# Kernel tuning notes

Hardware: AMD Instinct MI355X
Metric: run time of the kernel (lower is better)

Reference implementation:

```python
import jax, jax.numpy as jnp
import numpy as np

NUM_USERS = 100000
NUM_ITEMS = 200000
EMB_DIM = 64
N_LAYERS = 3
NNZ = 10000000
BATCH = 8192
N = NUM_USERS + NUM_ITEMS


def setup_inputs() -> dict:
    key = jax.random.key(0)
    k = jax.random.split(key, 7)
    return {
        "user_emb": jax.random.normal(k[0], (NUM_USERS, EMB_DIM), dtype=jnp.float32) * 0.05,
        "item_emb": jax.random.normal(k[1], (NUM_ITEMS, EMB_DIM), dtype=jnp.float32) * 0.05,
        "adj_vals": jax.random.uniform(k[2], (NNZ,), dtype=jnp.float32) * 0.01,
        "adj_rows": jax.random.randint(k[3], (NNZ,), 0, N, dtype=jnp.int32),
        "adj_cols": jax.random.randint(k[4], (NNZ,), 0, N, dtype=jnp.int32),
        "u_idx": jax.random.randint(k[5], (BATCH,), 0, NUM_USERS, dtype=jnp.int32),
        "i_idx": jax.random.randint(k[6], (BATCH,), 0, NUM_ITEMS, dtype=jnp.int32),
    }


def reference(user_emb, item_emb, adj_vals, adj_rows, adj_cols, u_idx, i_idx):
    # x0: [N, d] stacked user+item embeddings
    x0 = jnp.concatenate([user_emb, item_emb], axis=0)
    acc = x0
    x = x0
    for _ in range(N_LAYERS):
        # SpMM via gather + scaled scatter-add: y[r] += v * x[c]
        msg = adj_vals[:, None] * x[adj_cols]          # [nnz, d]
        x = jax.ops.segment_sum(msg, adj_rows, num_segments=N)
        acc = acc + x
    out = acc / jnp.float32(N_LAYERS + 1)              # mean over layer outputs
    u_all = out[:NUM_USERS]
    i_all = out[NUM_USERS:]
    # score(u_idx, i_idx): dot product of gathered final embeddings
    return jnp.sum(u_all[u_idx] * i_all[i_idx], axis=-1)  # [BATCH]
```

## Files before the change

kernel.cpp:

```cpp
#include <hip/hip_runtime.h>

#define NUM_USERS 100000
#define NUM_ITEMS 200000
#define EMB_DIM   64
#define NNODES    (NUM_USERS + NUM_ITEMS)
#define NNZ_C     10000000
#define BATCH_C   8192

typedef unsigned long long u64;

__device__ __forceinline__ u64 pack_edge(int c, float v) {
    return (u64)(unsigned int)c | ((u64)__float_as_uint(v) << 32);
}

__device__ __forceinline__ unsigned short f2bf(float f) {
    unsigned u = __float_as_uint(f);
    u += 0x7fffu + ((u >> 16) & 1u);
    return (unsigned short)(u >> 16);
}
__device__ __forceinline__ float bf2f(unsigned short h) {
    return __uint_as_float((unsigned)h << 16);
}

__global__ void zero_int_kernel(int* __restrict__ p, int n) {
    int i = blockIdx.x * blockDim.x + threadIdx.x;
    if (i < n) p[i] = 0;
}

__global__ void zero_f32_kernel(float* __restrict__ p, long long n) {
    long long i = (long long)blockIdx.x * blockDim.x + threadIdx.x;
    long long stride = (long long)gridDim.x * blockDim.x;
    for (; i < n; i += stride) p[i] = 0.f;
}

__global__ void convert_x0_kernel(const float* __restrict__ uemb,
                                  const float* __restrict__ iemb,
                                  ushort* __restrict__ x0) {
    const long long total4 = (long long)NNODES * EMB_DIM / 4;
    const long long usr4   = (long long)NUM_USERS * EMB_DIM / 4;
    long long g = (long long)blockIdx.x * blockDim.x + threadIdx.x;
    long long stride = (long long)gridDim.x * blockDim.x;
    for (; g < total4; g += stride) {
        long long base = g * 4;
        const float* src = (g < usr4) ? (uemb + base)
                                      : (iemb + (base - (long long)NUM_USERS * EMB_DIM));
        float4 v = *reinterpret_cast<const float4*>(src);
        ushort4 o = make_ushort4(f2bf(v.x), f2bf(v.y), f2bf(v.z), f2bf(v.w));
        *reinterpret_cast<ushort4*>(x0 + base) = o;
    }
}

__global__ void hist_kernel(const int* __restrict__ rows, int* __restrict__ cnt) {
    int i = blockIdx.x * blockDim.x + threadIdx.x;
    int stride = gridDim.x * blockDim.x;
    for (; i < NNZ_C; i += stride) {
        atomicAdd(&cnt[__builtin_nontemporal_load(rows + i)], 1);
    }
}

__global__ void scan_a(const int* __restrict__ cnt, int* __restrict__ rp,
                       int* __restrict__ bsum) {
    __shared__ int sm[256];
    int t = threadIdx.x;
    int base = blockIdx.x * 1024 + t * 4;
    int v0 = (base + 0 < NNODES) ? cnt[base + 0] : 0;
    int v1 = (base + 1 < NNODES) ? cnt[base + 1] : 0;
    int v2 = (base + 2 < NNODES) ? cnt[base + 2] : 0;
    int v3 = (base + 3 < NNODES) ? cnt[base + 3] : 0;
    int s = v0 + v1 + v2 + v3;
    sm[t] = s;
    __syncthreads();
    for (int off = 1; off < 256; off <<= 1) {
        int val = (t >= off) ? sm[t - off] : 0;
        __syncthreads();
        sm[t] += val;
        __syncthreads();
    }
    int incl = sm[t];
    int excl = incl - s;
    if (base + 0 < NNODES) rp[base + 0] = excl;
    if (base + 1 < NNODES) rp[base + 1] = excl + v0;
    if (base + 2 < NNODES) rp[base + 2] = excl + v0 + v1;
    if (base + 3 < NNODES) rp[base + 3] = excl + v0 + v1 + v2;
    if (t == 255) bsum[blockIdx.x] = incl;
}

__global__ void scan_b(int* __restrict__ bsum, int nblk) {
    __shared__ int sm[512];
    int t = threadIdx.x;
    int v = (t < nblk) ? bsum[t] : 0;
    sm[t] = v;
    __syncthreads();
    for (int off = 1; off < 512; off <<= 1) {
        int val = (t >= off) ? sm[t - off] : 0;
        __syncthreads();
        sm[t] += val;
        __syncthreads();
    }
    int excl = sm[t] - v;
    if (t < nblk) bsum[t] = excl;
}

__global__ void scan_c(int* __restrict__ rp, const int* __restrict__ bsum,
                       int* __restrict__ cursor) {
    int i = blockIdx.x * blockDim.x + threadIdx.x;
    if (i < NNODES) {
        int v = rp[i] + bsum[i >> 10];
        rp[i] = v;
        cursor[i] = v;
    }
    if (i == 0) rp[NNODES] = NNZ_C;
}

__global__ void scatter_kernel(const int* __restrict__ rows,
                               const int* __restrict__ cols,
                               const float* __restrict__ vals,
                               int* __restrict__ cursor,
                               u64* __restrict__ ccv) {
    int i = blockIdx.x * blockDim.x + threadIdx.x;
    int stride = gridDim.x * blockDim.x;
    for (; i < NNZ_C; i += stride) {
        int r = __builtin_nontemporal_load(rows + i);
        int c = __builtin_nontemporal_load(cols + i);
        float v = __builtin_nontemporal_load(vals + i);
        int pos = atomicAdd(&cursor[r], 1);
        ccv[pos] = pack_edge(c, v);
    }
}

template <bool ACCUM>
__global__ __launch_bounds__(256) void spmm_bf_kernel(
        const int* __restrict__ row_ptr, const u64* __restrict__ ccv,
        const ushort* __restrict__ xin, ushort* __restrict__ xout) {
    int row = blockIdx.x * 16 + (threadIdx.x >> 4);
    int lane = threadIdx.x & 63;
    int dl = lane & 15;
    int base = lane & 48;

    int start = row_ptr[row];
    int end   = row_ptr[row + 1];

    float ax = 0.f, ay = 0.f, az = 0.f, aw = 0.f;

    int cur = start;
    for (; cur + 16 <= end; cur += 16) {
        u64 e = __builtin_nontemporal_load(ccv + cur + dl);
        int   c = (int)(unsigned int)(e & 0xffffffffu);
        float v = __uint_as_float((unsigned int)(e >> 32));
#pragma unroll
        for (int j = 0; j < 16; ++j) {
            int   cj = __shfl(c, base + j);
            float vj = __shfl(v, base + j);
            ushort4 xb = *reinterpret_cast<const ushort4*>(
                xin + (size_t)cj * EMB_DIM + dl * 4);
            ax += vj * bf2f(xb.x);
            ay += vj * bf2f(xb.y);
            az += vj * bf2f(xb.z);
            aw += vj * bf2f(xb.w);
        }
    }
    int n = end - cur;
    if (n > 0) {
        int   c = 0;
        float v = 0.f;
        if (dl < n) {
            u64 e = ccv[cur + dl];
            c = (int)(unsigned int)(e & 0xffffffffu);
            v = __uint_as_float((unsigned int)(e >> 32));
        }
        for (int j = 0; j < n; ++j) {
            int   cj = __shfl(c, base + j);
            float vj = __shfl(v, base + j);
            ushort4 xb = *reinterpret_cast<const ushort4*>(
                xin + (size_t)cj * EMB_DIM + dl * 4);
            ax += vj * bf2f(xb.x);
            ay += vj * bf2f(xb.y);
            az += vj * bf2f(xb.z);
            aw += vj * bf2f(xb.w);
        }
    }

    ushort4* o = reinterpret_cast<ushort4*>(xout + (size_t)row * EMB_DIM) + dl;
    if (ACCUM) {
        ushort4 old = *o;
        ax += bf2f(old.x); ay += bf2f(old.y); az += bf2f(old.z); aw += bf2f(old.w);
    }
    *o = make_ushort4(f2bf(ax), f2bf(ay), f2bf(az), f2bf(aw));
}

template <bool FIRST>
__global__ __launch_bounds__(256) void coo_spmm_kernel(
        const int* __restrict__ rows, const int* __restrict__ cols,
        const float* __restrict__ vals, const float* __restrict__ xin,
        const float* __restrict__ uemb, const float* __restrict__ iemb,
        float* __restrict__ xout) {
    long long e = (long long)blockIdx.x * 16 + (threadIdx.x >> 4);
    int dl = threadIdx.x & 15;
    if (e >= NNZ_C) return;
    int r = rows[e];
    int c = cols[e];
    float v = vals[e];
    const float* src;
    if (FIRST) {
        src = (c < NUM_USERS) ? (uemb + (size_t)c * EMB_DIM)
                              : (iemb + (size_t)(c - NUM_USERS) * EMB_DIM);
    } else {
        src = xin + (size_t)c * EMB_DIM;
    }
    float4 xv = *reinterpret_cast<const float4*>(src + dl * 4);
    float* dst = xout + (size_t)r * EMB_DIM + dl * 4;
    atomicAdd(dst + 0, v * xv.x);
    atomicAdd(dst + 1, v * xv.y);
    atomicAdd(dst + 2, v * xv.z);
    atomicAdd(dst + 3, v * xv.w);
}

__global__ __launch_bounds__(256) void dot_bf_kernel(
        const float* __restrict__ uemb, const float* __restrict__ iemb,
        const ushort* __restrict__ A, const ushort* __restrict__ B,
        const int* __restrict__ u_idx, const int* __restrict__ i_idx,
        float* __restrict__ out) {
    int t = blockIdx.x * blockDim.x + threadIdx.x;
    int b = t >> 4;
    int dl = t & 15;
    if (b >= BATCH_C) return;

    int u = u_idx[b];
    int ii = i_idx[b];
    size_t uoff  = (size_t)u * EMB_DIM + dl * 4;
    size_t ioff  = (size_t)ii * EMB_DIM + dl * 4;
    size_t Aioff = (size_t)(NUM_USERS + ii) * EMB_DIM + dl * 4;

    float4 e_u = *reinterpret_cast<const float4*>(uemb + uoff);
    float4 e_i = *reinterpret_cast<const float4*>(iemb + ioff);
    ushort4 a_u = *reinterpret_cast<const ushort4*>(A + uoff);
    ushort4 b_u = *reinterpret_cast<const ushort4*>(B + uoff);
    ushort4 a_i = *reinterpret_cast<const ushort4*>(A + Aioff);
    ushort4 b_i = *reinterpret_cast<const ushort4*>(B + Aioff);

    float ux = e_u.x + bf2f(a_u.x) + bf2f(b_u.x);
    float uy = e_u.y + bf2f(a_u.y) + bf2f(b_u.y);
    float uz = e_u.z + bf2f(a_u.z) + bf2f(b_u.z);
    float uw = e_u.w + bf2f(a_u.w) + bf2f(b_u.w);
    float ix = e_i.x + bf2f(a_i.x) + bf2f(b_i.x);
    float iy = e_i.y + bf2f(a_i.y) + bf2f(b_i.y);
    float iz = e_i.z + bf2f(a_i.z) + bf2f(b_i.z);
    float iw = e_i.w + bf2f(a_i.w) + bf2f(b_i.w);

    float s = ux * ix + uy * iy + uz * iz + uw * iw;
    s += __shfl_xor(s, 1);
    s += __shfl_xor(s, 2);
    s += __shfl_xor(s, 4);
    s += __shfl_xor(s, 8);
    if (dl == 0) out[b] = s * 0.0625f;
}

__global__ __launch_bounds__(256) void dot_f32_kernel(
        const float* __restrict__ uemb, const float* __restrict__ iemb,
        const float* __restrict__ A, const float* __restrict__ B,
        const int* __restrict__ u_idx, const int* __restrict__ i_idx,
        float* __restrict__ out) {
    int t = blockIdx.x * blockDim.x + threadIdx.x;
    int b = t >> 4;
    int dl = t & 15;
    if (b >= BATCH_C) return;

    int u = u_idx[b];
    int ii = i_idx[b];
    size_t uoff  = (size_t)u * EMB_DIM + dl * 4;
    size_t ioff  = (size_t)ii * EMB_DIM + dl * 4;
    size_t Aioff = (size_t)(NUM_USERS + ii) * EMB_DIM + dl * 4;

    float4 e_u = *reinterpret_cast<const float4*>(uemb + uoff);
    float4 a_u = *reinterpret_cast<const float4*>(A + uoff);
    float4 b_u = *reinterpret_cast<const float4*>(B + uoff);
    float4 e_i = *reinterpret_cast<const float4*>(iemb + ioff);
    float4 a_i = *reinterpret_cast<const float4*>(A + Aioff);
    float4 b_i = *reinterpret_cast<const float4*>(B + Aioff);

    float ux = e_u.x + a_u.x + b_u.x, uy = e_u.y + a_u.y + b_u.y;
    float uz = e_u.z + a_u.z + b_u.z, uw = e_u.w + a_u.w + b_u.w;
    float ix = e_i.x + a_i.x + b_i.x, iy = e_i.y + a_i.y + b_i.y;
    float iz = e_i.z + a_i.z + b_i.z, iw = e_i.w + a_i.w + b_i.w;

    float s = ux * ix + uy * iy + uz * iz + uw * iw;
    s += __shfl_xor(s, 1);
    s += __shfl_xor(s, 2);
    s += __shfl_xor(s, 4);
    s += __shfl_xor(s, 8);
    if (dl == 0) out[b] = s * 0.0625f;
}

extern "C" void kernel_launch(void* const* d_in, const int* in_sizes, int n_in,
                              void* d_out, int out_size, void* d_ws, size_t ws_size,
                              hipStream_t stream) {
    const float* uemb     = (const float*)d_in[0];
    const float* iemb     = (const float*)d_in[1];
    const float* adj_vals = (const float*)d_in[2];
    const int*   adj_rows = (const int*)d_in[3];
    const int*   adj_cols = (const int*)d_in[4];
    const int*   u_idx    = (const int*)d_in[5];
    const int*   i_idx    = (const int*)d_in[6];
    float* out = (float*)d_out;
    (void)in_sizes; (void)n_in; (void)out_size;

    const size_t DENSE_BF = (size_t)NNODES * EMB_DIM * 2;
    const size_t DENSE_F32 = (size_t)NNODES * EMB_DIM * 4;
    const size_t ALIGN  = 256;
    auto rnd = [&](size_t b) { return (b + ALIGN - 1) & ~(ALIGN - 1); };

    const size_t need_full = rnd(DENSE_BF) * 3 + rnd((size_t)NNZ_C * 8) +
                             rnd((size_t)(NNODES + 1) * 4) + rnd((size_t)NNODES * 4) +
                             rnd(1024 * 4);
    const size_t need_min  = rnd(DENSE_F32) * 2;

    const long long dense_elems = (long long)NNODES * EMB_DIM;
    const int dot_grid = (BATCH_C * 16 + 255) / 256;

    if (ws_size >= need_full) {
        size_t off = 0;
        auto alloc = [&](size_t bytes) -> void* {
            void* p = (char*)d_ws + off;
            off += rnd(bytes);
            return p;
        };
        ushort* X0      = (ushort*)alloc(DENSE_BF);
        ushort* A       = (ushort*)alloc(DENSE_BF);
        ushort* B       = (ushort*)alloc(DENSE_BF);
        u64*    ccv     = (u64*)   alloc((size_t)NNZ_C * 8);
        int*    row_ptr = (int*)   alloc((size_t)(NNODES + 1) * 4);
        int*    cursor  = (int*)   alloc((size_t)NNODES * 4);
        int*    bsum    = (int*)   alloc(1024 * 4);

        const int nblk_scan = (NNODES + 1023) / 1024;

        zero_int_kernel<<<(NNODES + 255) / 256, 256, 0, stream>>>(cursor, NNODES);
        convert_x0_kernel<<<2048, 256, 0, stream>>>(uemb, iemb, X0);
        hist_kernel<<<2048, 256, 0, stream>>>(adj_rows, cursor);
        scan_a<<<nblk_scan, 256, 0, stream>>>(cursor, row_ptr, bsum);
        scan_b<<<1, 512, 0, stream>>>(bsum, nblk_scan);
        scan_c<<<(NNODES + 255) / 256, 256, 0, stream>>>(row_ptr, bsum, cursor);
        scatter_kernel<<<2048, 256, 0, stream>>>(adj_rows, adj_cols, adj_vals,
                                                 cursor, ccv);

        const int spmm_grid = NNODES / 16;
        spmm_bf_kernel<false><<<spmm_grid, 256, 0, stream>>>(row_ptr, ccv, X0, A);
        spmm_bf_kernel<false><<<spmm_grid, 256, 0, stream>>>(row_ptr, ccv, A, B);
        spmm_bf_kernel<true ><<<spmm_grid, 256, 0, stream>>>(row_ptr, ccv, B, A);

        dot_bf_kernel<<<dot_grid, 256, 0, stream>>>(uemb, iemb, A, B, u_idx, i_idx, out);
    } else if (ws_size >= need_min) {
        float* A = (float*)d_ws;
        float* B = (float*)((char*)d_ws + rnd(DENSE_F32));
        const int coo_grid = (NNZ_C + 15) / 16;

        zero_f32_kernel<<<2048, 256, 0, stream>>>(A, dense_elems);
        coo_spmm_kernel<true ><<<coo_grid, 256, 0, stream>>>(adj_rows, adj_cols, adj_vals,
                                                             nullptr, uemb, iemb, A);
        zero_f32_kernel<<<2048, 256, 0, stream>>>(B, dense_elems);
        coo_spmm_kernel<false><<<coo_grid, 256, 0, stream>>>(adj_rows, adj_cols, adj_vals,
                                                             A, nullptr, nullptr, B);
        coo_spmm_kernel<false><<<coo_grid, 256, 0, stream>>>(adj_rows, adj_cols, adj_vals,
                                                             B, nullptr, nullptr, A);

        dot_f32_kernel<<<dot_grid, 256, 0, stream>>>(uemb, iemb, A, B, u_idx, i_idx, out);
    }
}
```

Measured before the change: 1.650 ms.

## Build CSR via two-level bucketed counting sort with partitioned bucket counters

```diff
diff --git a/kernel.cpp b/kernel.cpp
--- a/kernel.cpp
+++ b/kernel.cpp
@@ -7,11 +7,13 @@
 #define NNZ_C     10000000
 #define BATCH_C   8192
 
+#define NBUCK     4688
+#define NPART     8
+#define NSEG      (NBUCK * NPART)
+#define SCAT_GRID 2048
+#define SCAN_ITEMS 37
+
 typedef unsigned long long u64;
-
-__device__ __forceinline__ u64 pack_edge(int c, float v) {
-    return (u64)(unsigned int)c | ((u64)__float_as_uint(v) << 32);
-}
 
 __device__ __forceinline__ unsigned short f2bf(float f) {
     unsigned u = __float_as_uint(f);
@@ -26,7 +28,6 @@
     int i = blockIdx.x * blockDim.x + threadIdx.x;
     if (i < n) p[i] = 0;
 }
-
 __global__ void zero_f32_kernel(float* __restrict__ p, long long n) {
     long long i = (long long)blockIdx.x * blockDim.x + threadIdx.x;
     long long stride = (long long)gridDim.x * blockDim.x;
@@ -45,86 +46,106 @@
         const float* src = (g < usr4) ? (uemb + base)
                                       : (iemb + (base - (long long)NUM_USERS * EMB_DIM));
         float4 v = *reinterpret_cast<const float4*>(src);
-        ushort4 o = make_ushort4(f2bf(v.x), f2bf(v.y), f2bf(v.z), f2bf(v.w));
-        *reinterpret_cast<ushort4*>(x0 + base) = o;
-    }
-}
-
-__global__ void hist_kernel(const int* __restrict__ rows, int* __restrict__ cnt) {
+        *reinterpret_cast<ushort4*>(x0 + base) =
+            make_ushort4(f2bf(v.x), f2bf(v.y), f2bf(v.z), f2bf(v.w));
+    }
+}
+
+__global__ void bucket_hist_kernel(const int* __restrict__ rows,
+                                   int* __restrict__ cnt) {
+    int p = blockIdx.x & (NPART - 1);
     int i = blockIdx.x * blockDim.x + threadIdx.x;
     int stride = gridDim.x * blockDim.x;
     for (; i < NNZ_C; i += stride) {
-        atomicAdd(&cnt[__builtin_nontemporal_load(rows + i)], 1);
-    }
-}
-
-__global__ void scan_a(const int* __restrict__ cnt, int* __restrict__ rp,
-                       int* __restrict__ bsum) {
-    __shared__ int sm[256];
+        int r = __builtin_nontemporal_load(rows + i);
+        atomicAdd(&cnt[(r >> 6) * NPART + p], 1);
+    }
+}
+
+__global__ __launch_bounds__(1024) void bucket_scan_kernel(
+        const int* __restrict__ cnt, int* __restrict__ base,
+        int* __restrict__ cur) {
+    __shared__ int sm[1024];
     int t = threadIdx.x;
-    int base = blockIdx.x * 1024 + t * 4;
-    int v0 = (base + 0 < NNODES) ? cnt[base + 0] : 0;
-    int v1 = (base + 1 < NNODES) ? cnt[base + 1] : 0;
-    int v2 = (base + 2 < NNODES) ? cnt[base + 2] : 0;
-    int v3 = (base + 3 < NNODES) ? cnt[base + 3] : 0;
-    int s = v0 + v1 + v2 + v3;
+    int first = t * SCAN_ITEMS;
+    int v[SCAN_ITEMS];
+    int s = 0;
+#pragma unroll
+    for (int k = 0; k < SCAN_ITEMS; ++k) {
+        int idx = first + k;
+        v[k] = (idx < NSEG) ? cnt[idx] : 0;
+        s += v[k];
+    }
     sm[t] = s;
     __syncthreads();
-    for (int off = 1; off < 256; off <<= 1) {
+    for (int off = 1; off < 1024; off <<= 1) {
         int val = (t >= off) ? sm[t - off] : 0;
         __syncthreads();
         sm[t] += val;
         __syncthreads();
     }
-    int incl = sm[t];
-    int excl = incl - s;
-    if (base + 0 < NNODES) rp[base + 0] = excl;
-    if (base + 1 < NNODES) rp[base + 1] = excl + v0;
-    if (base + 2 < NNODES) rp[base + 2] = excl + v0 + v1;
-    if (base + 3 < NNODES) rp[base + 3] = excl + v0 + v1 + v2;
-    if (t == 255) bsum[blockIdx.x] = incl;
-}
-
-__global__ void scan_b(int* __restrict__ bsum, int nblk) {
-    __shared__ int sm[512];
-    int t = threadIdx.x;
-    int v = (t < nblk) ? bsum[t] : 0;
-    sm[t] = v;
-    __syncthreads();
-    for (int off = 1; off < 512; off <<= 1) {
-        int val = (t >= off) ? sm[t - off] : 0;
-        __syncthreads();
-        sm[t] += val;
-        __syncthreads();
-    }
-    int excl = sm[t] - v;
-    if (t < nblk) bsum[t] = excl;
-}
-
-__global__ void scan_c(int* __restrict__ rp, const int* __restrict__ bsum,
-                       int* __restrict__ cursor) {
-    int i = blockIdx.x * blockDim.x + threadIdx.x;
-    if (i < NNODES) {
-        int v = rp[i] + bsum[i >> 10];
-        rp[i] = v;
-        cursor[i] = v;
-    }
-    if (i == 0) rp[NNODES] = NNZ_C;
-}
-
-__global__ void scatter_kernel(const int* __restrict__ rows,
-                               const int* __restrict__ cols,
-                               const float* __restrict__ vals,
-                               int* __restrict__ cursor,
-                               u64* __restrict__ ccv) {
+    int run = sm[t] - s;
+#pragma unroll
+    for (int k = 0; k < SCAN_ITEMS; ++k) {
+        int idx = first + k;
+        if (idx < NSEG) { base[idx] = run; cur[idx] = run; run += v[k]; }
+    }
+    if (t == 0) base[NSEG] = NNZ_C;
+}
+
+__global__ void bucket_scatter_kernel(const int* __restrict__ rows,
+                                      const int* __restrict__ cols,
+                                      const float* __restrict__ vals,
+                                      int* __restrict__ cur,
+                                      u64* __restrict__ tmp) {
+    int p = blockIdx.x & (NPART - 1);
     int i = blockIdx.x * blockDim.x + threadIdx.x;
     int stride = gridDim.x * blockDim.x;
     for (; i < NNZ_C; i += stride) {
-        int r = __builtin_nontemporal_load(rows + i);
-        int c = __builtin_nontemporal_load(cols + i);
+        int r   = __builtin_nontemporal_load(rows + i);
+        int c   = __builtin_nontemporal_load(cols + i);
         float v = __builtin_nontemporal_load(vals + i);
-        int pos = atomicAdd(&cursor[r], 1);
-        ccv[pos] = pack_edge(c, v);
+        int pos = atomicAdd(&cur[(r >> 6) * NPART + p], 1);
+        u64 rec = (u64)((unsigned)c | ((unsigned)(r & 63) << 19)) |
+                  ((u64)__float_as_uint(v) << 32);
+        tmp[pos] = rec;
+    }
+}
+
+__global__ __launch_bounds__(256) void csr_finalize_kernel(
+        const u64* __restrict__ tmp, const int* __restrict__ base,
+        int* __restrict__ row_ptr, u64* __restrict__ ccv) {
+    int b = blockIdx.x;
+    int s = base[b * NPART];
+    int e = base[b * NPART + NPART];
+    int t = threadIdx.x;
+
+    __shared__ int cnt[64];
+    __shared__ int off[64];
+    __shared__ int cur[64];
+
+    if (t < 64) cnt[t] = 0;
+    __syncthreads();
+    for (int i = s + t; i < e; i += 256) {
+        int rl = (int)((tmp[i] >> 19) & 63);
+        atomicAdd(&cnt[rl], 1);
+    }
+    __syncthreads();
+    if (t == 0) {
+        int acc = 0;
+        for (int r = 0; r < 64; ++r) { off[r] = acc; acc += cnt[r]; }
+    }
+    __syncthreads();
+    int brow = b * 64;
+    if (t < 64 && brow + t < NNODES) row_ptr[brow + t] = s + off[t];
+    if (b == 0 && t == 0) row_ptr[NNODES] = NNZ_C;
+    if (t < 64) cur[t] = s + off[t];
+    __syncthreads();
+    for (int i = s + t; i < e; i += 256) {
+        u64 v = tmp[i];
+        int rl = (int)((v >> 19) & 63);
+        int pos = atomicAdd(&cur[rl], 1);
+        ccv[pos] = (v & 0xffffffff00000000ull) | (v & 0x7ffffull);
     }
 }
 
@@ -304,14 +325,15 @@
     float* out = (float*)d_out;
     (void)in_sizes; (void)n_in; (void)out_size;
 
-    const size_t DENSE_BF = (size_t)NNODES * EMB_DIM * 2;
+    const size_t DENSE_BF  = (size_t)NNODES * EMB_DIM * 2;
     const size_t DENSE_F32 = (size_t)NNODES * EMB_DIM * 4;
-    const size_t ALIGN  = 256;
+    const size_t EDGES     = (size_t)NNZ_C * 8;
+    const size_t ALIGN = 256;
     auto rnd = [&](size_t b) { return (b + ALIGN - 1) & ~(ALIGN - 1); };
 
-    const size_t need_full = rnd(DENSE_BF) * 3 + rnd((size_t)NNZ_C * 8) +
-                             rnd((size_t)(NNODES + 1) * 4) + rnd((size_t)NNODES * 4) +
-                             rnd(1024 * 4);
+    const size_t region0 = rnd(DENSE_BF * 3 > EDGES ? DENSE_BF * 3 : EDGES);
+    const size_t need_full = region0 + rnd(EDGES) + rnd((size_t)(NNODES + 1) * 4) +
+                             rnd((size_t)(NSEG + 1) * 4) * 3;
     const size_t need_min  = rnd(DENSE_F32) * 2;
 
     const long long dense_elems = (long long)NNODES * EMB_DIM;
@@ -324,25 +346,26 @@
             off += rnd(bytes);
             return p;
         };
-        ushort* X0      = (ushort*)alloc(DENSE_BF);
-        ushort* A       = (ushort*)alloc(DENSE_BF);
-        ushort* B       = (ushort*)alloc(DENSE_BF);
-        u64*    ccv     = (u64*)   alloc((size_t)NNZ_C * 8);
-        int*    row_ptr = (int*)   alloc((size_t)(NNODES + 1) * 4);
-        int*    cursor  = (int*)   alloc((size_t)NNODES * 4);
-        int*    bsum    = (int*)   alloc(1024 * 4);
-
-        const int nblk_scan = (NNODES + 1023) / 1024;
-
-        zero_int_kernel<<<(NNODES + 255) / 256, 256, 0, stream>>>(cursor, NNODES);
+        char*  r0      = (char*)alloc(region0);
+        u64*   ccv     = (u64*) alloc(EDGES);
+        int*   row_ptr = (int*) alloc((size_t)(NNODES + 1) * 4);
+        int*   bbase   = (int*) alloc((size_t)(NSEG + 1) * 4);
+        int*   bcur    = (int*) alloc((size_t)(NSEG + 1) * 4);
+        int*   bcnt    = (int*) alloc((size_t)(NSEG + 1) * 4);
+
+        u64*    tmp = (u64*)r0;
+        ushort* X0  = (ushort*)r0;
+        ushort* A   = X0 + dense_elems;
+        ushort* B   = A + dense_elems;
+
+        zero_int_kernel<<<(NSEG + 255) / 256, 256, 0, stream>>>(bcnt, NSEG);
+        bucket_hist_kernel<<<SCAT_GRID, 256, 0, stream>>>(adj_rows, bcnt);
+        bucket_scan_kernel<<<1, 1024, 0, stream>>>(bcnt, bbase, bcur);
+        bucket_scatter_kernel<<<SCAT_GRID, 256, 0, stream>>>(adj_rows, adj_cols,
+                                                             adj_vals, bcur, tmp);
+        csr_finalize_kernel<<<NBUCK, 256, 0, stream>>>(tmp, bbase, row_ptr, ccv);
+
         convert_x0_kernel<<<2048, 256, 0, stream>>>(uemb, iemb, X0);
-        hist_kernel<<<2048, 256, 0, stream>>>(adj_rows, cursor);
-        scan_a<<<nblk_scan, 256, 0, stream>>>(cursor, row_ptr, bsum);
-        scan_b<<<1, 512, 0, stream>>>(bsum, nblk_scan);
-        scan_c<<<(NNODES + 255) / 256, 256, 0, stream>>>(row_ptr, bsum, cursor);
-        scatter_kernel<<<2048, 256, 0, stream>>>(adj_rows, adj_cols, adj_vals,
-                                                 cursor, ccv);
-
         const int spmm_grid = NNODES / 16;
         spmm_bf_kernel<false><<<spmm_grid, 256, 0, stream>>>(row_ptr, ccv, X0, A);
         spmm_bf_kernel<false><<<spmm_grid, 256, 0, stream>>>(row_ptr, ccv, A, B);
```

After: 1.694 ms. +2.6%, slower.
